# Kernel optimization log

Hardware: AMD Instinct MI355X
Metric: run time of the kernel (lower is better)

Reference implementation:

```python
import jax, jax.numpy as jnp
import numpy as np

NUM_HEADS = 16
D_MODEL = 2048
HEAD_DIM = 128
ROPE_BASE = 10000


def setup_inputs() -> dict:
    key = jax.random.key(0)
    k1, k2, k3 = jax.random.split(key, 3)
    B, S = 2, 2048
    x = jax.random.normal(k1, (B, S, D_MODEL), dtype=jnp.float32)
    attn_mask = jnp.ones((B, S), dtype=jnp.int32)
    in_proj = 0.02 * jax.random.normal(k2, (3, D_MODEL, NUM_HEADS, HEAD_DIM), dtype=jnp.float32)
    out_proj = 0.02 * jax.random.normal(k3, (NUM_HEADS, HEAD_DIM, D_MODEL), dtype=jnp.float32)
    return {"x": x, "attn_mask": attn_mask, "in_proj": in_proj, "out_proj": out_proj}


def _rope(t, seq_len):
    # t: [B, S, H, hd]; faithful to RotaryEmbedding.__call__ (concat layout, not interleaved)
    half = HEAD_DIM // 2
    inv_freq = 1.0 / (ROPE_BASE ** (2 * jnp.arange(0, half, dtype=jnp.float32) / HEAD_DIM))
    positions = jnp.arange(seq_len, dtype=jnp.float32)
    angles = positions[:, None] * inv_freq[None, :]            # [S, hd/2]
    cos = jnp.cos(angles)[None, :, None, :]                    # [1, S, 1, hd/2]
    sin = jnp.sin(angles)[None, :, None, :]
    tr = t.reshape(*t.shape[:-1], half, 2)                     # [B,S,H,hd/2,2]
    t0, t1 = tr[..., 0], tr[..., 1]
    out = jnp.concatenate([t0 * cos - t1 * sin, t0 * sin + t1 * cos], axis=-1)
    return out.reshape(t.shape)


def reference(x, attn_mask, in_proj, out_proj):
    B, S, D = x.shape
    qkv = jnp.einsum('bsd,tdhm->tbshm', x, in_proj)            # fused QKV
    q, k, v = qkv[0], qkv[1], qkv[2]
    q = _rope(q, S)
    k = _rope(k, S)
    q = jnp.einsum('bshd->bhsd', q)
    k = jnp.einsum('bshd->bhsd', k)
    v = jnp.einsum('bshd->bhsd', v)
    scores = jnp.einsum('bhqd,bhkd->bhqk', q, k) / jnp.sqrt(jnp.float32(HEAD_DIM))
    # causal mask * key padding mask, with diagonal forced to 1
    causal = jnp.tril(jnp.ones((S, S), dtype=scores.dtype))    # [S,S]
    key_mask = attn_mask.astype(scores.dtype)[:, None, :]      # [B,1,S]
    combined = causal[None, :, :] * key_mask                   # [B,S,S]
    eye = jnp.eye(S, dtype=bool)
    combined = jnp.where(eye[None, :, :], jnp.asarray(1.0, scores.dtype), combined)
    scores = scores + (-(1.0 - combined) * 1e9)[:, None, :, :]  # broadcast over heads
    attn_weights = jax.nn.softmax(scores, axis=-1)
    return jnp.einsum('bhqk,bhkd,hdo->bqo', attn_weights, v, out_proj)
```

## Files before the change

kernel.cpp:

```cpp
#include <hip/hip_runtime.h>
#include <hip/hip_bf16.h>

#define B_   2
#define S_   2048
#define H_   16
#define HD_  128
#define D_   2048
#define BS_  4096
#define SCALE_ 0.08838834764831845f

typedef __hip_bfloat16 bf16;
typedef float f32x4 __attribute__((ext_vector_type(4)));
typedef __bf16 bf16x8 __attribute__((ext_vector_type(8)));
typedef unsigned short u16x8 __attribute__((ext_vector_type(8)));
typedef unsigned short u16x4 __attribute__((ext_vector_type(4)));

static __device__ __forceinline__ unsigned short f2bf_u(float f) {
  bf16 h = __float2bfloat16(f);
  return __builtin_bit_cast(unsigned short, h);
}
static __device__ __forceinline__ void load_lds16(const void* g, void* l) {
  __builtin_amdgcn_global_load_lds((const __attribute__((address_space(1))) void*)g,
                                   (__attribute__((address_space(3))) void*)l, 16, 0, 0);
}

__global__ __launch_bounds__(256) void k_convert(const float* __restrict__ src,
                                                 bf16* __restrict__ dst) {
  const size_t i = ((size_t)blockIdx.x * 256 + threadIdx.x) * 8;
  const float4 a = *(const float4*)(src + i);
  const float4 b = *(const float4*)(src + i + 4);
  u16x8 o;
  o[0] = f2bf_u(a.x); o[1] = f2bf_u(a.y); o[2] = f2bf_u(a.z); o[3] = f2bf_u(a.w);
  o[4] = f2bf_u(b.x); o[5] = f2bf_u(b.y); o[6] = f2bf_u(b.z); o[7] = f2bf_u(b.w);
  *(u16x8*)(dst + i) = o;
}

__global__ __launch_bounds__(256) void k_transpose(const float* __restrict__ src0,
                                                   bf16* __restrict__ dst0) {
  const int z = blockIdx.z;
  const float* src = src0 + (size_t)z * D_ * D_;
  bf16* dst = dst0 + (size_t)z * D_ * D_;
  __shared__ float tile[64][65];
  const int t = threadIdx.x;
  const int x0 = blockIdx.x * 64, y0 = blockIdx.y * 64;
#pragma unroll
  for (int i = 0; i < 16; ++i) {
    int idx = t + i * 256, r = idx >> 6, c = idx & 63;
    tile[r][c] = src[(size_t)(y0 + r) * D_ + x0 + c];
  }
  __syncthreads();
#pragma unroll
  for (int i = 0; i < 16; ++i) {
    int idx = t + i * 256, c = idx >> 6, r = idx & 63;
    dst[(size_t)(x0 + c) * D_ + y0 + r] = __float2bfloat16(tile[r][c]);
  }
}

__global__ __launch_bounds__(256) void k_rope_tables(float* __restrict__ cost,
                                                     float* __restrict__ sint) {
  const int idx = blockIdx.x * 256 + threadIdx.x;
  const int s = idx >> 6, d = idx & 63;
  const float inv = expf(-(float)d * (9.210340371976184f / 64.f));
  const float ang = (float)s * inv;
  cost[idx] = cosf(ang);
  sint[idx] = sinf(ang);
}

template <int MODE>
__global__ __launch_bounds__(512, 4) void k_gemm_p(const bf16* __restrict__ A,
                                                   const bf16* __restrict__ Bt,
                                                   float* __restrict__ Cf,
                                                   bf16* __restrict__ qb,
                                                   bf16* __restrict__ kb,
                                                   bf16* __restrict__ vt,
                                                   const float* __restrict__ cost,
                                                   const float* __restrict__ sint) {
  constexpr int BN = (MODE == 1) ? 128 : 256;
  constexpr int NF = BN / 64;
  constexpr int BSTRIDE = 8192 + BN * 64;
  extern __shared__ __align__(16) char smem[];
  const int tid = threadIdx.x;
  const int w = tid >> 6, lane = tid & 63;
  const int wm = w >> 2, wn = w & 3;
  const int lr = lane & 15, lg = lane >> 4;
  const int brow = blockIdx.x * 128, bcol = blockIdx.y * BN;

  f32x4 acc[4][NF] = {};

  auto stage = [&](int kt, int buf) {
    char* base = smem + buf * BSTRIDE;
    {
      const int row = tid >> 2, su = tid & 3;
      const int up = su ^ ((row >> 1) & 3);
      load_lds16(A + (size_t)(brow + row) * D_ + kt * 32 + up * 8, base + w * 1024);
    }
#pragma unroll
    for (int i = 0; i < BN / 128; ++i) {
      const int slot = i * 512 + tid;
      const int row = slot >> 2, su = slot & 3;
      const int up = su ^ ((row >> 1) & 3);
      load_lds16(Bt + (size_t)(bcol + row) * D_ + kt * 32 + up * 8,
                 base + 8192 + i * 8192 + w * 1024);
    }
  };

  const int NKT = D_ / 32;
  stage(0, 0); stage(1, 1);
  int bs = 0;
  for (int kt = 0; kt < NKT; ++kt) {
    if (kt < NKT - 1) {
      if constexpr (MODE == 1) asm volatile("s_waitcnt vmcnt(2)" ::: "memory");
      else                     asm volatile("s_waitcnt vmcnt(3)" ::: "memory");
    } else {
      asm volatile("s_waitcnt vmcnt(0)" ::: "memory");
    }
    __builtin_amdgcn_s_barrier();
    __builtin_amdgcn_sched_barrier(0);
    if (kt + 2 < NKT) {
      int sb = bs + 2; if (sb >= 3) sb -= 3;
      stage(kt + 2, sb);
    }

    const char* base = smem + bs * BSTRIDE;
    bf16x8 af[4], bf4[NF];
#pragma unroll
    for (int q = 0; q < 4; ++q) {
      const int r = wm * 64 + q * 16 + lr;
      af[q] = *(const bf16x8*)(base + r * 64 + ((lg ^ ((r >> 1) & 3)) * 16));
    }
#pragma unroll
    for (int nf = 0; nf < NF; ++nf) {
      const int r = wn * (NF * 16) + nf * 16 + lr;
      bf4[nf] = *(const bf16x8*)(base + 8192 + r * 64 + ((lg ^ ((r >> 1) & 3)) * 16));
    }
    __builtin_amdgcn_s_setprio(1);
#pragma unroll
    for (int q = 0; q < 4; ++q)
#pragma unroll
      for (int nf = 0; nf < NF; ++nf)
        acc[q][nf] = __builtin_amdgcn_mfma_f32_16x16x32_bf16(af[q], bf4[nf], acc[q][nf], 0, 0, 0);
    __builtin_amdgcn_s_setprio(0);
    bs = (bs == 2) ? 0 : bs + 1;
  }

  if (MODE == 1) {
#pragma unroll
    for (int mf = 0; mf < 4; ++mf)
#pragma unroll
      for (int nf = 0; nf < NF; ++nf) {
        const int col = bcol + wn * (NF * 16) + nf * 16 + lr;
#pragma unroll
        for (int j = 0; j < 4; ++j) {
          const int row = brow + wm * 64 + mf * 16 + lg * 4 + j;
          Cf[(size_t)row * D_ + col] = acc[mf][nf][j];
        }
      }
  } else {
    const int t = bcol >> 11;
#pragma unroll
    for (int mf = 0; mf < 4; ++mf)
#pragma unroll
      for (int nf = 0; nf < NF; ++nf) {
        const int col = bcol + wn * (NF * 16) + nf * 16 + lr;
        const int h = (col >> 7) & (H_ - 1), mm = col & (HD_ - 1);
        if (t == 2) {
          const int row0 = brow + wm * 64 + mf * 16 + lg * 4;
          const int b = row0 >> 11, s0 = row0 & (S_ - 1);
          u16x4 pk;
#pragma unroll
          for (int j = 0; j < 4; ++j) pk[j] = f2bf_u(acc[mf][nf][j]);
          *(u16x4*)(vt + ((size_t)(b * H_ + h) * HD_ + mm) * S_ + s0) = pk;
        } else {
          const int i2 = mm >> 1;
          const bool odd = mm & 1;
#pragma unroll
          for (int j = 0; j < 4; ++j) {
            const int row = brow + wm * 64 + mf * 16 + lg * 4 + j;
            const int b = row >> 11, s = row & (S_ - 1);
            const float val = acc[mf][nf][j];
            const float part = __shfl_xor(val, 1, 64);
            const float c = cost[s * 64 + i2];
            const float sn = sint[s * 64 + i2];
            float o = odd ? (part * sn + val * c) : (val * c - part * sn);
            if (t == 0) o *= SCALE_;
            const int om = odd ? (64 + i2) : i2;
            bf16* dst = (t == 1) ? kb : qb;
            dst[((size_t)(b * H_ + h) * S_ + s) * HD_ + om] = __float2bfloat16(o);
          }
        }
      }
  }
}

__global__ __launch_bounds__(256, 2) void k_attn(const bf16* __restrict__ qb,
                                                 const bf16* __restrict__ kb,
                                                 const bf16* __restrict__ vt,
                                                 const int* __restrict__ mask,
                                                 bf16* __restrict__ attn_b) {
  const int tid = threadIdx.x, w = tid >> 6, lane = tid & 63;
  const int lr = lane & 15, lg = lane >> 4;
  const int qt = (blockIdx.y < 16) ? ((int)gridDim.x - 1 - (int)blockIdx.x)
                                   : (int)blockIdx.x;
  const int q0 = qt * 128;
  const int bh = blockIdx.y;
  const int b = bh >> 4, h = bh & (H_ - 1);
  const bf16* qp = qb + (size_t)bh * S_ * HD_;
  const bf16* kp = kb + (size_t)bh * S_ * HD_;
  const bf16* vp = vt + (size_t)bh * HD_ * S_;
  __shared__ __align__(16) bf16 Ks[2][64 * 128];
  __shared__ __align__(16) bf16 Vs[2][128 * 64];
  __shared__ __align__(16) bf16 Ps[4][16][80];

  const int qrowA = q0 + w * 16 + lr;
  bf16x8 qfA[4], qfB[4];
#pragma unroll
  for (int ks = 0; ks < 4; ++ks) {
    qfA[ks] = *(const bf16x8*)(qp + (size_t)qrowA * HD_ + ks * 32 + lg * 8);
    qfB[ks] = *(const bf16x8*)(qp + (size_t)(qrowA + 64) * HD_ + ks * 32 + lg * 8);
  }

  float mA[4], lA[4], mB[4], lB[4];
  f32x4 oA[8], oB[8];
#pragma unroll
  for (int j = 0; j < 4; ++j) { mA[j] = -INFINITY; lA[j] = 0.f; mB[j] = -INFINITY; lB[j] = 0.f; }
#pragma unroll
  for (int c = 0; c < 8; ++c) { oA[c] = (f32x4)(0.f); oB[c] = (f32x4)(0.f); }

  auto stage = [&](int buf, int k0) {
#pragma unroll
    for (int i = 0; i < 4; ++i) {
      const int slot = i * 256 + tid;
      const int row = slot >> 4, j16 = slot & 15;
      load_lds16(kp + (size_t)(k0 + row) * HD_ + ((j16 ^ (row & 7)) * 8),
                 (char*)&Ks[buf][0] + i * 4096 + w * 1024);
    }
#pragma unroll
    for (int i = 0; i < 4; ++i) {
      const int slot = i * 256 + tid;
      const int row = slot >> 3, j8 = slot & 7;
      load_lds16(vp + (size_t)row * S_ + k0 + ((j8 ^ (row & 7)) * 8),
                 (char*)&Vs[buf][0] + i * 4096 + w * 1024);
    }
  };

  auto sm_pv = [&](f32x4 (&sacc)[4], float (&m_run)[4], float (&l_run)[4],
                   f32x4 (&oacc)[8], const int rbase, const int k0,
                   const int (&mk4)[4], const bf16* vsb) {
    float mblk[4] = {-INFINITY, -INFINITY, -INFINITY, -INFINITY};
#pragma unroll
    for (int n = 0; n < 4; ++n) {
      const int kcol = k0 + n * 16 + lr;
#pragma unroll
      for (int j = 0; j < 4; ++j) {
        const int r = rbase + lg * 4 + j;
        float sv = sacc[n][j];
        const bool allowed = (kcol <= r) && (mk4[n] != 0 || kcol == r);
        sv = allowed ? sv : -1e9f;
        sacc[n][j] = sv;
        mblk[j] = fmaxf(mblk[j], sv);
      }
    }
#pragma unroll
    for (int xm = 1; xm < 16; xm <<= 1)
#pragma unroll
      for (int j = 0; j < 4; ++j)
        mblk[j] = fmaxf(mblk[j], __shfl_xor(mblk[j], xm, 64));

    bool grow = false;
#pragma unroll
    for (int j = 0; j < 4; ++j) grow = grow || (mblk[j] > m_run[j] + 8.f);
    if (__any(grow)) {
      float alpha[4];
#pragma unroll
      for (int j = 0; j < 4; ++j) {
        const float mn = fmaxf(m_run[j], mblk[j]);
        alpha[j] = __expf(m_run[j] - mn);
        m_run[j] = mn;
        l_run[j] *= alpha[j];
      }
#pragma unroll
      for (int c = 0; c < 8; ++c)
#pragma unroll
        for (int j = 0; j < 4; ++j) oacc[c][j] *= alpha[j];
    }

    float psum[4] = {0.f, 0.f, 0.f, 0.f};
#pragma unroll
    for (int n = 0; n < 4; ++n)
#pragma unroll
      for (int j = 0; j < 4; ++j) {
        const float p = __expf(sacc[n][j] - m_run[j]);
        psum[j] += p;
        sacc[n][j] = p;
      }
#pragma unroll
    for (int xm = 1; xm < 16; xm <<= 1)
#pragma unroll
      for (int j = 0; j < 4; ++j)
        psum[j] += __shfl_xor(psum[j], xm, 64);
#pragma unroll
    for (int j = 0; j < 4; ++j) l_run[j] += psum[j];

#pragma unroll
    for (int n = 0; n < 4; ++n)
#pragma unroll
      for (int j = 0; j < 4; ++j)
        Ps[w][lg * 4 + j][n * 16 + lr] = __float2bfloat16(sacc[n][j]);

    bf16x8 pa[2];
#pragma unroll
    for (int ks = 0; ks < 2; ++ks)
      pa[ks] = *(const bf16x8*)(&Ps[w][lr][ks * 32 + lg * 8]);
    __builtin_amdgcn_s_setprio(1);
#pragma unroll
    for (int c = 0; c < 8; ++c) {
#pragma unroll
      for (int ks = 0; ks < 2; ++ks) {
        const int vrow = c * 16 + lr;
        const int unit = (ks * 4 + lg) ^ (vrow & 7);
        const bf16x8 vf = *(const bf16x8*)(vsb + vrow * 64 + unit * 8);
        oacc[c] = __builtin_amdgcn_mfma_f32_16x16x32_bf16(pa[ks], vf, oacc[c], 0, 0, 0);
      }
    }
    __builtin_amdgcn_s_setprio(0);
  };

  const int nt = 2 * qt + 2;
  stage(0, 0);
  asm volatile("s_waitcnt vmcnt(0)" ::: "memory");
  __syncthreads();

  int cur = 0;
  for (int it = 0; it < nt; ++it) {
    const int k0 = it * 64;
    if (it + 1 < nt) stage(cur ^ 1, k0 + 64);

    int mk4[4];
#pragma unroll
    for (int n = 0; n < 4; ++n) mk4[n] = mask[b * S_ + k0 + n * 16 + lr];

    const bf16* ksb = &Ks[cur][0];
    const bf16* vsb = &Vs[cur][0];

    f32x4 sA[4] = {}, sB[4] = {};
    __builtin_amdgcn_s_setprio(1);
#pragma unroll
    for (int n = 0; n < 4; ++n) {
      const int krow = n * 16 + lr;
#pragma unroll
      for (int ks = 0; ks < 4; ++ks) {
        const int j16 = (ks * 4 + lg) ^ (krow & 7);
        const bf16x8 kf = *(const bf16x8*)(ksb + krow * 128 + j16 * 8);
        sA[n] = __builtin_amdgcn_mfma_f32_16x16x32_bf16(qfA[ks], kf, sA[n], 0, 0, 0);
        sB[n] = __builtin_amdgcn_mfma_f32_16x16x32_bf16(qfB[ks], kf, sB[n], 0, 0, 0);
      }
    }
    __builtin_amdgcn_s_setprio(0);

    sm_pv(sA, mA, lA, oA, q0 + w * 16, k0, mk4, vsb);
    sm_pv(sB, mB, lB, oB, q0 + 64 + w * 16, k0, mk4, vsb);

    asm volatile("s_waitcnt vmcnt(0)" ::: "memory");
    __syncthreads();
    cur ^= 1;
  }

#pragma unroll
  for (int j = 0; j < 4; ++j) {
    const float invA = 1.f / lA[j];
    const float invB = 1.f / lB[j];
    const int rA = q0 + w * 16 + lg * 4 + j;
#pragma unroll
    for (int c = 0; c < 8; ++c) {
      attn_b[(size_t)(b * S_ + rA) * D_ + h * HD_ + c * 16 + lr] =
          __float2bfloat16(oA[c][j] * invA);
      attn_b[(size_t)(b * S_ + rA + 64) * D_ + h * HD_ + c * 16 + lr] =
          __float2bfloat16(oB[c][j] * invB);
    }
  }
}

extern "C" void kernel_launch(void* const* d_in, const int* in_sizes, int n_in,
                              void* d_out, int out_size, void* d_ws, size_t ws_size,
                              hipStream_t stream) {
  (void)in_sizes; (void)n_in; (void)out_size; (void)ws_size;
  const float* x        = (const float*)d_in[0];
  const int*   attn_mask= (const int*)d_in[1];
  const float* in_proj  = (const float*)d_in[2];
  const float* out_proj = (const float*)d_in[3];
  float* out = (float*)d_out;
  char* ws = (char*)d_ws;

  bf16*  xb    = (bf16*)(ws + 0);
  bf16*  wqkvT = (bf16*)(ws + 16777216);
  bf16*  woT   = (bf16*)(ws + 41943040);
  float* cost  = (float*)(ws + 50331648);
  float* sint  = (float*)(ws + 50855936);
  bf16*  vt    = (bf16*)(ws + 51380224);
  bf16* qb = (bf16*)d_out;
  bf16* kb = (bf16*)((char*)d_out + 16777216);
  bf16* attn_b = xb;

  static int lds_ok = 0;
  if (!lds_ok) {
    (void)hipFuncSetAttribute((const void*)k_gemm_p<0>,
                              hipFuncAttributeMaxDynamicSharedMemorySize, 73728);
    (void)hipFuncSetAttribute((const void*)k_gemm_p<1>,
                              hipFuncAttributeMaxDynamicSharedMemorySize, 49152);
    lds_ok = 1;
  }

  k_convert<<<4096, 256, 0, stream>>>(x, xb);
  k_transpose<<<dim3(32, 32, 3), 256, 0, stream>>>(in_proj, wqkvT);
  k_transpose<<<dim3(32, 32, 1), 256, 0, stream>>>(out_proj, woT);
  k_rope_tables<<<512, 256, 0, stream>>>(cost, sint);
  k_gemm_p<0><<<dim3(32, 24), 512, 73728, stream>>>(xb, wqkvT, nullptr, qb, kb, vt, cost, sint);
  k_attn<<<dim3(16, 32), 256, 0, stream>>>(qb, kb, vt, attn_mask, attn_b);
  k_gemm_p<1><<<dim3(32, 16), 512, 49152, stream>>>(attn_b, woT, out, nullptr, nullptr, nullptr,
                                                    nullptr, nullptr);
}
```

Measured before the change: 306.0 us.

## Split attention work across eight waves, one 16-row query tile each

```diff
diff --git a/kernel.cpp b/kernel.cpp
--- a/kernel.cpp
+++ b/kernel.cpp
@@ -192,7 +192,7 @@
   }
 }
 
-__global__ __launch_bounds__(256, 2) void k_attn(const bf16* __restrict__ qb,
+__global__ __launch_bounds__(512, 4) void k_attn(const bf16* __restrict__ qb,
                                                  const bf16* __restrict__ kb,
                                                  const bf16* __restrict__ vt,
                                                  const int* __restrict__ mask,
@@ -209,120 +209,36 @@
   const bf16* vp = vt + (size_t)bh * HD_ * S_;
   __shared__ __align__(16) bf16 Ks[2][64 * 128];
   __shared__ __align__(16) bf16 Vs[2][128 * 64];
-  __shared__ __align__(16) bf16 Ps[4][16][80];
-
-  const int qrowA = q0 + w * 16 + lr;
-  bf16x8 qfA[4], qfB[4];
-#pragma unroll
-  for (int ks = 0; ks < 4; ++ks) {
-    qfA[ks] = *(const bf16x8*)(qp + (size_t)qrowA * HD_ + ks * 32 + lg * 8);
-    qfB[ks] = *(const bf16x8*)(qp + (size_t)(qrowA + 64) * HD_ + ks * 32 + lg * 8);
-  }
-
-  float mA[4], lA[4], mB[4], lB[4];
-  f32x4 oA[8], oB[8];
-#pragma unroll
-  for (int j = 0; j < 4; ++j) { mA[j] = -INFINITY; lA[j] = 0.f; mB[j] = -INFINITY; lB[j] = 0.f; }
-#pragma unroll
-  for (int c = 0; c < 8; ++c) { oA[c] = (f32x4)(0.f); oB[c] = (f32x4)(0.f); }
+  __shared__ __align__(16) bf16 Ps[8][16][40];
+
+  const int qrow = q0 + w * 16 + lr;
+  bf16x8 qf[4];
+#pragma unroll
+  for (int ks = 0; ks < 4; ++ks)
+    qf[ks] = *(const bf16x8*)(qp + (size_t)qrow * HD_ + ks * 32 + lg * 8);
+
+  float m_run[4], l_run[4];
+  f32x4 oacc[8];
+#pragma unroll
+  for (int j = 0; j < 4; ++j) { m_run[j] = -INFINITY; l_run[j] = 0.f; }
+#pragma unroll
+  for (int c = 0; c < 8; ++c) oacc[c] = (f32x4)(0.f);
 
   auto stage = [&](int buf, int k0) {
 #pragma unroll
-    for (int i = 0; i < 4; ++i) {
-      const int slot = i * 256 + tid;
+    for (int i = 0; i < 2; ++i) {
+      const int slot = i * 512 + tid;
       const int row = slot >> 4, j16 = slot & 15;
       load_lds16(kp + (size_t)(k0 + row) * HD_ + ((j16 ^ (row & 7)) * 8),
-                 (char*)&Ks[buf][0] + i * 4096 + w * 1024);
-    }
-#pragma unroll
-    for (int i = 0; i < 4; ++i) {
-      const int slot = i * 256 + tid;
+                 (char*)&Ks[buf][0] + i * 8192 + w * 1024);
+    }
+#pragma unroll
+    for (int i = 0; i < 2; ++i) {
+      const int slot = i * 512 + tid;
       const int row = slot >> 3, j8 = slot & 7;
       load_lds16(vp + (size_t)row * S_ + k0 + ((j8 ^ (row & 7)) * 8),
-                 (char*)&Vs[buf][0] + i * 4096 + w * 1024);
-    }
-  };
-
-  auto sm_pv = [&](f32x4 (&sacc)[4], float (&m_run)[4], float (&l_run)[4],
-                   f32x4 (&oacc)[8], const int rbase, const int k0,
-                   const int (&mk4)[4], const bf16* vsb) {
-    float mblk[4] = {-INFINITY, -INFINITY, -INFINITY, -INFINITY};
-#pragma unroll
-    for (int n = 0; n < 4; ++n) {
-      const int kcol = k0 + n * 16 + lr;
-#pragma unroll
-      for (int j = 0; j < 4; ++j) {
-        const int r = rbase + lg * 4 + j;
-        float sv = sacc[n][j];
-        const bool allowed = (kcol <= r) && (mk4[n] != 0 || kcol == r);
-        sv = allowed ? sv : -1e9f;
-        sacc[n][j] = sv;
-        mblk[j] = fmaxf(mblk[j], sv);
-      }
-    }
-#pragma unroll
-    for (int xm = 1; xm < 16; xm <<= 1)
-#pragma unroll
-      for (int j = 0; j < 4; ++j)
-        mblk[j] = fmaxf(mblk[j], __shfl_xor(mblk[j], xm, 64));
-
-    bool grow = false;
-#pragma unroll
-    for (int j = 0; j < 4; ++j) grow = grow || (mblk[j] > m_run[j] + 8.f);
-    if (__any(grow)) {
-      float alpha[4];
-#pragma unroll
-      for (int j = 0; j < 4; ++j) {
-        const float mn = fmaxf(m_run[j], mblk[j]);
-        alpha[j] = __expf(m_run[j] - mn);
-        m_run[j] = mn;
-        l_run[j] *= alpha[j];
-      }
-#pragma unroll
-      for (int c = 0; c < 8; ++c)
-#pragma unroll
-        for (int j = 0; j < 4; ++j) oacc[c][j] *= alpha[j];
-    }
-
-    float psum[4] = {0.f, 0.f, 0.f, 0.f};
-#pragma unroll
-    for (int n = 0; n < 4; ++n)
-#pragma unroll
-      for (int j = 0; j < 4; ++j) {
-        const float p = __expf(sacc[n][j] - m_run[j]);
-        psum[j] += p;
-        sacc[n][j] = p;
-      }
-#pragma unroll
-    for (int xm = 1; xm < 16; xm <<= 1)
-#pragma unroll
-      for (int j = 0; j < 4; ++j)
-        psum[j] += __shfl_xor(psum[j], xm, 64);
-#pragma unroll
-    for (int j = 0; j < 4; ++j) l_run[j] += psum[j];
-
-#pragma unroll
-    for (int n = 0; n < 4; ++n)
-#pragma unroll
-      for (int j = 0; j < 4; ++j)
-        Ps[w][lg * 4 + j][n * 16 + lr] = __float2bfloat16(sacc[n][j]);
-
-    bf16x8 pa[2];
-#pragma unroll
-    for (int ks = 0; ks < 2; ++ks)
-      pa[ks] = *(const bf16x8*)(&Ps[w][lr][ks * 32 + lg * 8]);
-    __builtin_amdgcn_s_setprio(1);
-#pragma unroll
-    for (int c = 0; c < 8; ++c) {
-#pragma unroll
-      for (int ks = 0; ks < 2; ++ks) {
-        const int vrow = c * 16 + lr;
-        const int unit = (ks * 4 + lg) ^ (vrow & 7);
-        const bf16x8 vf = *(const bf16x8*)(vsb + vrow * 64 + unit * 8);
-        oacc[c] = __builtin_amdgcn_mfma_f32_16x16x32_bf16(pa[ks], vf, oacc[c], 0, 0, 0);
-      }
-    }
-    __builtin_amdgcn_s_setprio(0);
+                 (char*)&Vs[buf][0] + i * 8192 + w * 1024);
+    }
   };
 
   const int nt = 2 * qt + 2;
@@ -335,30 +251,104 @@
     const int k0 = it * 64;
     if (it + 1 < nt) stage(cur ^ 1, k0 + 64);
 
-    int mk4[4];
-#pragma unroll
-    for (int n = 0; n < 4; ++n) mk4[n] = mask[b * S_ + k0 + n * 16 + lr];
-
-    const bf16* ksb = &Ks[cur][0];
-    const bf16* vsb = &Vs[cur][0];
-
-    f32x4 sA[4] = {}, sB[4] = {};
-    __builtin_amdgcn_s_setprio(1);
-#pragma unroll
-    for (int n = 0; n < 4; ++n) {
-      const int krow = n * 16 + lr;
-#pragma unroll
-      for (int ks = 0; ks < 4; ++ks) {
-        const int j16 = (ks * 4 + lg) ^ (krow & 7);
-        const bf16x8 kf = *(const bf16x8*)(ksb + krow * 128 + j16 * 8);
-        sA[n] = __builtin_amdgcn_mfma_f32_16x16x32_bf16(qfA[ks], kf, sA[n], 0, 0, 0);
-        sB[n] = __builtin_amdgcn_mfma_f32_16x16x32_bf16(qfB[ks], kf, sB[n], 0, 0, 0);
-      }
-    }
-    __builtin_amdgcn_s_setprio(0);
-
-    sm_pv(sA, mA, lA, oA, q0 + w * 16, k0, mk4, vsb);
-    sm_pv(sB, mB, lB, oB, q0 + 64 + w * 16, k0, mk4, vsb);
+    const bool active = (it + 1 < nt) || (w >= 4);
+
+    if (active) {
+      int mk4[4];
+#pragma unroll
+      for (int n = 0; n < 4; ++n) mk4[n] = mask[b * S_ + k0 + n * 16 + lr];
+
+      const bf16* ksb = &Ks[cur][0];
+      const bf16* vsb = &Vs[cur][0];
+
+      f32x4 sacc[4] = {};
+      __builtin_amdgcn_s_setprio(1);
+#pragma unroll
+      for (int n = 0; n < 4; ++n) {
+        const int krow = n * 16 + lr;
+#pragma unroll
+        for (int ks = 0; ks < 4; ++ks) {
+          const int j16 = (ks * 4 + lg) ^ (krow & 7);
+          const bf16x8 kf = *(const bf16x8*)(ksb + krow * 128 + j16 * 8);
+          sacc[n] = __builtin_amdgcn_mfma_f32_16x16x32_bf16(qf[ks], kf, sacc[n], 0, 0, 0);
+        }
+      }
+      __builtin_amdgcn_s_setprio(0);
+
+      float mblk[4] = {-INFINITY, -INFINITY, -INFINITY, -INFINITY};
+#pragma unroll
+      for (int n = 0; n < 4; ++n) {
+        const int kcol = k0 + n * 16 + lr;
+#pragma unroll
+        for (int j = 0; j < 4; ++j) {
+          const int r = q0 + w * 16 + lg * 4 + j;
+          float sv = sacc[n][j];
+          const bool allowed = (kcol <= r) && (mk4[n] != 0 || kcol == r);
+          sv = allowed ? sv : -1e9f;
+          sacc[n][j] = sv;
+          mblk[j] = fmaxf(mblk[j], sv);
+        }
+      }
+#pragma unroll
+      for (int xm = 1; xm < 16; xm <<= 1)
+#pragma unroll
+        for (int j = 0; j < 4; ++j)
+          mblk[j] = fmaxf(mblk[j], __shfl_xor(mblk[j], xm, 64));
+
+      bool grow = false;
+#pragma unroll
+      for (int j = 0; j < 4; ++j) grow = grow || (mblk[j] > m_run[j] + 8.f);
+      if (__any(grow)) {
+        float alpha[4];
+#pragma unroll
+        for (int j = 0; j < 4; ++j) {
+          const float mn = fmaxf(m_run[j], mblk[j]);
+          alpha[j] = __expf(m_run[j] - mn);
+          m_run[j] = mn;
+          l_run[j] *= alpha[j];
+        }
+#pragma unroll
+        for (int c = 0; c < 8; ++c)
+#pragma unroll
+          for (int j = 0; j < 4; ++j) oacc[c][j] *= alpha[j];
+      }
+
+      float psum[4] = {0.f, 0.f, 0.f, 0.f};
+#pragma unroll
+      for (int n = 0; n < 4; ++n)
+#pragma unroll
+        for (int j = 0; j < 4; ++j) {
+          const float p = __expf(sacc[n][j] - m_run[j]);
+          psum[j] += p;
+          sacc[n][j] = p;
+        }
+#pragma unroll
+      for (int xm = 1; xm < 16; xm <<= 1)
+#pragma unroll
+        for (int j = 0; j < 4; ++j)
+          psum[j] += __shfl_xor(psum[j], xm, 64);
+#pragma unroll
+      for (int j = 0; j < 4; ++j) l_run[j] += psum[j];
+
+#pragma unroll
+      for (int hh = 0; hh < 2; ++hh) {
+#pragma unroll
+        for (int n2 = 0; n2 < 2; ++n2)
+#pragma unroll
+          for (int j = 0; j < 4; ++j)
+            Ps[w][lg * 4 + j][n2 * 16 + lr] = __float2bfloat16(sacc[hh * 2 + n2][j]);
+        const bf16x8 pa = *(const bf16x8*)(&Ps[w][lr][lg * 8]);
+        __builtin_amdgcn_s_setprio(1);
+#pragma unroll
+        for (int c = 0; c < 8; ++c) {
+          const int vrow = c * 16 + lr;
+          const int unit = (hh * 4 + lg) ^ (vrow & 7);
+          const bf16x8 vf = *(const bf16x8*)(vsb + vrow * 64 + unit * 8);
+          oacc[c] = __builtin_amdgcn_mfma_f32_16x16x32_bf16(pa, vf, oacc[c], 0, 0, 0);
+        }
+        __builtin_amdgcn_s_setprio(0);
+      }
+    }
 
     asm volatile("s_waitcnt vmcnt(0)" ::: "memory");
     __syncthreads();
@@ -367,16 +357,12 @@
 
 #pragma unroll
   for (int j = 0; j < 4; ++j) {
-    const float invA = 1.f / lA[j];
-    const float invB = 1.f / lB[j];
-    const int rA = q0 + w * 16 + lg * 4 + j;
-#pragma unroll
-    for (int c = 0; c < 8; ++c) {
-      attn_b[(size_t)(b * S_ + rA) * D_ + h * HD_ + c * 16 + lr] =
-          __float2bfloat16(oA[c][j] * invA);
-      attn_b[(size_t)(b * S_ + rA + 64) * D_ + h * HD_ + c * 16 + lr] =
-          __float2bfloat16(oB[c][j] * invB);
-    }
+    const float inv = 1.f / l_run[j];
+    const int r = q0 + w * 16 + lg * 4 + j;
+#pragma unroll
+    for (int c = 0; c < 8; ++c)
+      attn_b[(size_t)(b * S_ + r) * D_ + h * HD_ + c * 16 + lr] =
+          __float2bfloat16(oacc[c][j] * inv);
   }
 }
 
@@ -415,7 +401,7 @@
   k_transpose<<<dim3(32, 32, 1), 256, 0, stream>>>(out_proj, woT);
   k_rope_tables<<<512, 256, 0, stream>>>(cost, sint);
   k_gemm_p<0><<<dim3(32, 24), 512, 73728, stream>>>(xb, wqkvT, nullptr, qb, kb, vt, cost, sint);
-  k_attn<<<dim3(16, 32), 256, 0, stream>>>(qb, kb, vt, attn_mask, attn_b);
+  k_attn<<<dim3(16, 32), 512, 0, stream>>>(qb, kb, vt, attn_mask, attn_b);
   k_gemm_p<1><<<dim3(32, 16), 512, 49152, stream>>>(attn_b, woT, out, nullptr, nullptr, nullptr,
                                                     nullptr, nullptr);
 }
```

New measurement: 278.5 us. 9.0% less time.
